# Optimization experiments

Hardware: AMD Instinct MI355X
Metric: run time of the kernel (lower is better)

## Reference

```python
import jax, jax.numpy as jnp
import numpy as np

X_DIM, R_DIM, U_DIM, V_DIM, H_DIM = 64, 64, 64, 64, 128


def setup_inputs() -> dict:
    key = jax.random.key(0)
    k1, k2, k3, k4, k5 = jax.random.split(key, 5)
    n, i, j = 8, 32, 32
    r = jax.random.normal(k1, (n, i, j, R_DIM), dtype=jnp.float32)
    u = jax.random.normal(k2, (n, R_DIM, U_DIM, V_DIM), dtype=jnp.float32)
    v = jax.random.normal(k3, (n, i, j, V_DIM), dtype=jnp.float32)
    # xavier_uniform scaling: gain=1, fan computed over last two dims per torch default
    def xavier(k, shape):
        fan_in, fan_out = shape[-1], shape[-2]
        # torch xavier on >2D tensor: fan_in = shape[1]*prod(shape[2:]), fan_out = shape[0]*prod(shape[2:])
        rf = int(np.prod(shape[2:])) if len(shape) > 2 else 1
        fi = shape[1] * rf
        fo = shape[0] * rf
        bound = float(np.sqrt(6.0 / (fi + fo)))
        return jax.random.uniform(k, shape, dtype=jnp.float32, minval=-bound, maxval=bound)
    w1 = xavier(k4, (R_DIM, U_DIM, V_DIM, H_DIM))
    w2 = xavier(k5, (X_DIM, R_DIM, H_DIM))
    return {"r": r, "u": u, "v": v, "w1": w1, "w2": w2}


def reference(r, u, v, w1, w2):
    # contract w1 with u over (u_dim, v_dim) -> per-batch tensor a[n, r, v', h]
    # original: einsum('ruvh,nruv,nijv->nijrh')
    a = jnp.einsum('ruvh,nruv->nrvh', w1, u)          # contract u axis; v survives? no:
    # Careful: in 'ruvh,nruv,nijv->nijrh', v is contracted across all three.
    # Do it in two GEMM-friendly steps: first contract u-axis, keeping v.
    # a: [n, r, v, h] (contracted only over u)
    a = jnp.einsum('ruvh,nruv->nrvh', w1, u)
    # then contract v with v-tensor: [n,i,j,v] x [n,r,v,h] -> [n,i,j,r,h]
    x = jax.nn.relu(jnp.einsum('nijv,nrvh->nijrh', v, a))
    # second einsum: 'xrh,nijr,nijrh->nijx'
    # fuse r-weighting into x first (elementwise over r), then contract (r,h) with w2
    out = jnp.einsum('xrh,nijrh->nijx', w2, x * r[..., None])
    return out
```

## Files before the change

### kernel.cpp

```cpp
#include <hip/hip_runtime.h>
#include <hip/hip_bf16.h>

#define RD 64
#define UD 64
#define VD 64
#define HD 128
#define XD 64
#define NB 8
#define SITES 1024

typedef float f32x4 __attribute__((ext_vector_type(4)));
typedef float f32x2 __attribute__((ext_vector_type(2)));
typedef __bf16 bf16x4 __attribute__((ext_vector_type(4)));
typedef __bf16 bf16x8 __attribute__((ext_vector_type(8)));
typedef unsigned int u32x4 __attribute__((ext_vector_type(4)));
typedef unsigned short u16;
typedef unsigned short u16x4 __attribute__((ext_vector_type(4)));

__device__ __forceinline__ void lds_barrier() {
  __builtin_amdgcn_s_waitcnt(0xC07F);
  __builtin_amdgcn_s_barrier();
}

__global__ void kprep(const float* __restrict__ w2, u16* __restrict__ w2t,
                      const float* __restrict__ r, float* __restrict__ rt,
                      const float* __restrict__ u, float* __restrict__ ut) {
  __shared__ float tl[64][68];
  int b = blockIdx.x;
  int t = threadIdx.x;
  if (b < 256) {
    int rr = b >> 2, qq = b & 3;
    for (int i = 0; i < 8; ++i) {
      int idx = qq * 2048 + i * 256 + t;
      int x = idx >> 7, h = idx & 127;
      float val = w2[((size_t)x * RD + rr) * HD + h];
      __hip_bfloat16 hv = __float2bfloat16(val);
      w2t[((size_t)rr * XD + x) * HD + h] = *(u16*)&hv;
    }
  } else if (b < 384) {
    int bb = b - 256;
    int n = bb >> 4, sb = (bb & 15) * 64;
    for (int i = 0; i < 4; ++i) {
      int flat = i * 256 + t;
      int s = flat >> 4, ch = flat & 15;
      f32x4 d = *(const f32x4*)(r + ((size_t)(n * SITES + sb + s) * RD + ch * 4));
      *(f32x4*)&tl[s][ch * 4] = d;
    }
    __syncthreads();
    for (int i = 0; i < 4; ++i) {
      int flat = i * 256 + t;
      int rr = flat >> 4, ch = flat & 15;
      f32x4 o;
      o.x = tl[ch * 4 + 0][rr];
      o.y = tl[ch * 4 + 1][rr];
      o.z = tl[ch * 4 + 2][rr];
      o.w = tl[ch * 4 + 3][rr];
      *(f32x4*)(rt + ((size_t)(n * RD + rr) * SITES + sb + ch * 4)) = o;
    }
  } else {
    int f = (b - 384) * 256 + t;
    int nh = f & 1, v = (f >> 1) & 63, uu = (f >> 7) & 63, rr = f >> 13;
    f32x4 o;
#pragma unroll
    for (int k = 0; k < 4; ++k)
      o[k] = u[(((size_t)(nh * 4 + k) * RD + rr) * UD + uu) * VD + v];
    *(f32x4*)(ut + (size_t)f * 4) = o;
  }
}

#define PF 4
__global__ __launch_bounds__(512, 4) void k_a_full(const float* __restrict__ w1,
                                                   const float* __restrict__ ut,
                                                   u16* __restrict__ at) {
  __shared__ float red[256 * 32];
  __shared__ float tile[8 * 32 * 33];
  int b = blockIdx.x;
  int rr = b >> 3, vh = (b >> 2) & 1, hb = b & 3;
  int t = threadIdx.x;
  int uh = t >> 8;
  int L = t & 255;
  int vl = L >> 3, hs = L & 7;
  int v = vh * 32 + vl;
  int h0 = hb * 32 + hs * 4;
  const float* w1p = w1 + (((size_t)(rr * UD + uh * 32)) * VD + v) * HD + h0;
  const float* up  = ut + (((size_t)(rr * UD + uh * 32)) * VD + v) * NB;
  const size_t wstep = (size_t)VD * HD;
  const size_t ustep = (size_t)VD * NB;

  f32x4 acc[8];
#pragma unroll
  for (int n = 0; n < 8; ++n) acc[n] = (f32x4)0.f;

  f32x4 wa[PF], ua[PF], ub[PF];
#pragma unroll
  for (int p = 0; p < PF; ++p) {
    wa[p] = *(const f32x4*)(w1p + (size_t)p * wstep);
    ua[p] = *(const f32x4*)(up + (size_t)p * ustep);
    ub[p] = *(const f32x4*)(up + (size_t)p * ustep + 4);
  }
#pragma unroll
  for (int uu = 0; uu < 32; ++uu) {
    const int p = uu & (PF - 1);
    f32x4 wv = wa[p];
    f32x4 a0 = ua[p];
    f32x4 a1 = ub[p];
    if (uu + PF < 32) {
      wa[p] = *(const f32x4*)(w1p + (size_t)(uu + PF) * wstep);
      ua[p] = *(const f32x4*)(up + (size_t)(uu + PF) * ustep);
      ub[p] = *(const f32x4*)(up + (size_t)(uu + PF) * ustep + 4);
    }
    acc[0] += wv * a0.x;
    acc[1] += wv * a0.y;
    acc[2] += wv * a0.z;
    acc[3] += wv * a0.w;
    acc[4] += wv * a1.x;
    acc[5] += wv * a1.y;
    acc[6] += wv * a1.z;
    acc[7] += wv * a1.w;
  }

  if (uh == 1) {
#pragma unroll
    for (int n = 0; n < 8; ++n)
      *(f32x4*)&red[L * 32 + ((n ^ (L & 7)) << 2)] = acc[n];
  }
  __syncthreads();
  if (uh == 0) {
#pragma unroll
    for (int n = 0; n < 8; ++n)
      acc[n] += *(const f32x4*)&red[L * 32 + ((n ^ (L & 7)) << 2)];
#pragma unroll
    for (int n = 0; n < 8; ++n)
#pragma unroll
      for (int j = 0; j < 4; ++j)
        tile[(n * 32 + hs * 4 + j) * 33 + vl] = acc[n][j];
  }
  __syncthreads();

#pragma unroll
  for (int k = 0; k < 4; ++k) {
    int flat = k * 512 + t;
    int vs = flat & 7, hl = (flat >> 3) & 31, n = flat >> 8;
    f32x4 blk = *(const f32x4*)&tile[(n * 32 + hl) * 33 + vs * 4];
    u16x4 o;
#pragma unroll
    for (int j = 0; j < 4; ++j) {
      __hip_bfloat16 hv = __float2bfloat16(blk[j]);
      o[j] = *(u16*)&hv;
    }
    *(u16x4*)(at + ((size_t)(n * RD + rr) * HD + hb * 32 + hl) * VD + vh * 32 + vs * 4) = o;
  }
}

__global__ __launch_bounds__(256, 1) void k_main(const float* __restrict__ vin,
                                                 const u16* __restrict__ at,
                                                 const u16* __restrict__ w2t,
                                                 const float* __restrict__ rt,
                                                 float* __restrict__ pbuf) {
  __shared__ __align__(16) char Plds[2 * 128 * 256];
  int b = blockIdx.x;
  int rc = b & 7, st = (b >> 3) & 7, n = b >> 6;
  int t = threadIdx.x;
  int w = t >> 6, L = t & 63, q = L >> 4, c = L & 15;
  int g2m = w >> 1, g2x = w & 1;

  bf16x8 vf[4][2];
#pragma unroll
  for (int nt = 0; nt < 4; ++nt)
#pragma unroll
    for (int ks = 0; ks < 2; ++ks) {
      int s = (w & 1) * 64 + nt * 16 + c;
      const float* vp = vin + ((size_t)(n * SITES + st * 128 + s) * VD + ks * 32 + q * 8);
      f32x4 a0 = *(const f32x4*)vp;
      f32x4 a1 = *(const f32x4*)(vp + 4);
      bf16x8 f;
      f[0] = (__bf16)a0.x; f[1] = (__bf16)a0.y; f[2] = (__bf16)a0.z; f[3] = (__bf16)a0.w;
      f[4] = (__bf16)a1.x; f[5] = (__bf16)a1.y; f[6] = (__bf16)a1.z; f[7] = (__bf16)a1.w;
      vf[nt][ks] = f;
    }

  f32x4 o[4][2];
#pragma unroll
  for (int i = 0; i < 4; i++)
#pragma unroll
    for (int j = 0; j < 2; j++) o[i][j] = (f32x4)0.f;

  int g1m = w >> 1, g1n = w & 1;
  for (int rr = rc * 8; rr < rc * 8 + 8; ++rr) {
    const u16* abase = at + (size_t)(n * RD + rr) * 8192;

    bf16x8 af[4][2];
#pragma unroll
    for (int mt = 0; mt < 4; ++mt)
#pragma unroll
      for (int ks = 0; ks < 2; ++ks) {
        int h = g1m * 64 + mt * 16 + c;
        int vb = ks * 4 + q;
        af[mt][ks] = *(const bf16x8*)(abase + (size_t)h * VD + vb * 8);
      }
    u32x4 wraw[2][4];
#pragma unroll
    for (int xt = 0; xt < 2; ++xt)
#pragma unroll
      for (int k2 = 0; k2 < 4; ++k2) {
        int xg = g2x * 32 + xt * 16 + c;
        wraw[xt][k2] = *(const u32x4*)((const char*)w2t +
                        (((size_t)(rr * XD + xg)) * HD + k2 * 32 + q * 8) * 2);
      }
    float rsc[4];
#pragma unroll
    for (int nt = 0; nt < 4; ++nt)
      rsc[nt] = rt[(size_t)(n * RD + rr) * SITES + st * 128 + g1n * 64 + nt * 16 + c];

    f32x4 cc[4][4];
#pragma unroll
    for (int mt = 0; mt < 4; ++mt)
#pragma unroll
      for (int nt = 0; nt < 4; ++nt) cc[mt][nt] = (f32x4)0.f;
#pragma unroll
    for (int ks = 0; ks < 2; ++ks)
#pragma unroll
      for (int mt = 0; mt < 4; ++mt)
#pragma unroll
        for (int nt = 0; nt < 4; ++nt)
          cc[mt][nt] = __builtin_amdgcn_mfma_f32_16x16x32_bf16(af[mt][ks], vf[nt][ks],
                                                               cc[mt][nt], 0, 0, 0);

    char* PB = Plds + (rr & 1) * 32768;
#pragma unroll
    for (int mt = 0; mt < 4; ++mt)
#pragma unroll
      for (int nt = 0; nt < 4; ++nt) {
        float sc = rsc[nt];
        bf16x4 pv;
#pragma unroll
        for (int jj = 0; jj < 4; ++jj) {
          float x = cc[mt][nt][jj];
          x = x > 0.f ? x : 0.f;
          pv[jj] = (__bf16)(x * sc);
        }
        int s = g1n * 64 + nt * 16 + c;
        int blk = g1m * 8 + mt * 2 + (q >> 1);
        *(bf16x4*)(PB + (size_t)s * 256 + (size_t)((blk ^ c) * 16 + (q & 1) * 8)) = pv;
      }
    lds_barrier();

#pragma unroll
    for (int k2 = 0; k2 < 4; ++k2) {
      bf16x8 wf0 = __builtin_bit_cast(bf16x8, wraw[0][k2]);
      bf16x8 wf1 = __builtin_bit_cast(bf16x8, wraw[1][k2]);
#pragma unroll
      for (int mt = 0; mt < 4; ++mt) {
        int s = g2m * 64 + mt * 16 + c;
        int blk = k2 * 4 + q;
        bf16x8 pf = *(const bf16x8*)(PB + (size_t)s * 256 + (size_t)((blk ^ c) * 16));
        o[mt][0] = __builtin_amdgcn_mfma_f32_16x16x32_bf16(pf, wf0, o[mt][0], 0, 0, 0);
        o[mt][1] = __builtin_amdgcn_mfma_f32_16x16x32_bf16(pf, wf1, o[mt][1], 0, 0, 0);
      }
    }
  }
#pragma unroll
  for (int mt = 0; mt < 4; ++mt)
#pragma unroll
    for (int xt = 0; xt < 2; ++xt) {
      int s0 = g2m * 64 + mt * 16 + q * 4;
      int x = g2x * 32 + xt * 16 + c;
      size_t off = ((((size_t)rc * NB + n) * 8 + st) * XD + x) * 128 + s0;
      *(f32x4*)(pbuf + off) = o[mt][xt];
    }
}

__global__ __launch_bounds__(256) void k_reduce(const float* __restrict__ pbuf,
                                                float* __restrict__ out) {
  __shared__ float tile[128][17];
  int b = blockIdx.x;
  int n = b >> 5, st = (b >> 2) & 7, xq = b & 3;
  int t = threadIdx.x;
  int sq = t & 31, xl = t >> 5;
#pragma unroll
  for (int p = 0; p < 2; ++p) {
    int x = xq * 16 + p * 8 + xl;
    f32x4 sum = (f32x4)0.f;
#pragma unroll
    for (int rcc = 0; rcc < 8; ++rcc) {
      size_t off = ((((size_t)rcc * NB + n) * 8 + st) * XD + x) * 128 + sq * 4;
      f32x4 d = *(const f32x4*)(pbuf + off);
      sum.x += d.x; sum.y += d.y; sum.z += d.z; sum.w += d.w;
    }
#pragma unroll
    for (int k = 0; k < 4; ++k) tile[sq * 4 + k][p * 8 + xl] = sum[k];
  }
  __syncthreads();
#pragma unroll
  for (int k = 0; k < 2; ++k) {
    int flat = k * 256 + t;
    int s = flat >> 2, c4 = flat & 3;
    f32x4 o;
#pragma unroll
    for (int j = 0; j < 4; ++j) o[j] = tile[s][c4 * 4 + j];
    *(f32x4*)(out + ((size_t)(n * SITES + st * 128 + s) * XD + xq * 16 + c4 * 4)) = o;
  }
}

extern "C" void kernel_launch(void* const* d_in, const int* in_sizes, int n_in,
                              void* d_out, int out_size, void* d_ws, size_t ws_size,
                              hipStream_t stream) {
  const float* r  = (const float*)d_in[0];
  const float* u  = (const float*)d_in[1];
  const float* v  = (const float*)d_in[2];
  const float* w1 = (const float*)d_in[3];
  const float* w2 = (const float*)d_in[4];
  float* out = (float*)d_out;
  char* ws = (char*)d_ws;
  u16* at     = (u16*)(ws);
  u16* w2t    = (u16*)(ws + ((size_t)8 << 20));
  float* rt   = (float*)(ws + ((size_t)9 << 20));
  float* ut   = (float*)(ws + ((size_t)11 << 20));
  float* pbuf = (float*)(ws + ((size_t)19 << 20));

  hipLaunchKernelGGL(kprep, dim3(2432), dim3(256), 0, stream, w2, w2t, r, rt, u, ut);
  hipLaunchKernelGGL(k_a_full, dim3(512), dim3(512), 0, stream, w1, ut, at);
  hipLaunchKernelGGL(k_main, dim3(512), dim3(256), 0, stream, v, at, w2t, rt, pbuf);
  hipLaunchKernelGGL(k_reduce, dim3(256), dim3(256), 0, stream, pbuf, out);
}
```

Measured before the change: 255.3 us.

## Stage u slab in shared memory inside k_a_full instead of pre-transposing

```diff
diff --git a/kernel.cpp b/kernel.cpp
--- a/kernel.cpp
+++ b/kernel.cpp
@@ -23,8 +23,7 @@
 }
 
 __global__ void kprep(const float* __restrict__ w2, u16* __restrict__ w2t,
-                      const float* __restrict__ r, float* __restrict__ rt,
-                      const float* __restrict__ u, float* __restrict__ ut) {
+                      const float* __restrict__ r, float* __restrict__ rt) {
   __shared__ float tl[64][68];
   int b = blockIdx.x;
   int t = threadIdx.x;
@@ -37,7 +36,7 @@
       __hip_bfloat16 hv = __float2bfloat16(val);
       w2t[((size_t)rr * XD + x) * HD + h] = *(u16*)&hv;
     }
-  } else if (b < 384) {
+  } else {
     int bb = b - 256;
     int n = bb >> 4, sb = (bb & 15) * 64;
     for (int i = 0; i < 4; ++i) {
@@ -57,23 +56,14 @@
       o.w = tl[ch * 4 + 3][rr];
       *(f32x4*)(rt + ((size_t)(n * RD + rr) * SITES + sb + ch * 4)) = o;
     }
-  } else {
-    int f = (b - 384) * 256 + t;
-    int nh = f & 1, v = (f >> 1) & 63, uu = (f >> 7) & 63, rr = f >> 13;
-    f32x4 o;
-#pragma unroll
-    for (int k = 0; k < 4; ++k)
-      o[k] = u[(((size_t)(nh * 4 + k) * RD + rr) * UD + uu) * VD + v];
-    *(f32x4*)(ut + (size_t)f * 4) = o;
   }
 }
 
 #define PF 4
 __global__ __launch_bounds__(512, 4) void k_a_full(const float* __restrict__ w1,
-                                                   const float* __restrict__ ut,
+                                                   const float* __restrict__ u,
                                                    u16* __restrict__ at) {
-  __shared__ float red[256 * 32];
-  __shared__ float tile[8 * 32 * 33];
+  __shared__ __align__(16) float smem[16640];
   int b = blockIdx.x;
   int rr = b >> 3, vh = (b >> 2) & 1, hb = b & 3;
   int t = threadIdx.x;
@@ -82,43 +72,50 @@
   int vl = L >> 3, hs = L & 7;
   int v = vh * 32 + vl;
   int h0 = hb * 32 + hs * 4;
+
+  {
+    const float* ub = u + (size_t)rr * UD * VD + (size_t)vh * 32;
+#pragma unroll
+    for (int i = 0; i < 8; ++i) {
+      int s = i * 512 + t;
+      int n = s >> 9, uu = (s >> 3) & 63, vg = s & 7;
+      f32x4 d = *(const f32x4*)(ub + (size_t)n * (RD * UD * VD) + (size_t)uu * VD + vg * 4);
+      *(f32x4*)&smem[s * 4] = d;
+    }
+  }
+  __syncthreads();
+
   const float* w1p = w1 + (((size_t)(rr * UD + uh * 32)) * VD + v) * HD + h0;
-  const float* up  = ut + (((size_t)(rr * UD + uh * 32)) * VD + v) * NB;
   const size_t wstep = (size_t)VD * HD;
-  const size_t ustep = (size_t)VD * NB;
+  const float* uslab = smem + (size_t)uh * 32 * 32 + vl;
 
   f32x4 acc[8];
 #pragma unroll
   for (int n = 0; n < 8; ++n) acc[n] = (f32x4)0.f;
 
-  f32x4 wa[PF], ua[PF], ub[PF];
-#pragma unroll
-  for (int p = 0; p < PF; ++p) {
-    wa[p] = *(const f32x4*)(w1p + (size_t)p * wstep);
-    ua[p] = *(const f32x4*)(up + (size_t)p * ustep);
-    ub[p] = *(const f32x4*)(up + (size_t)p * ustep + 4);
-  }
-#pragma unroll
-  for (int uu = 0; uu < 32; ++uu) {
-    const int p = uu & (PF - 1);
+  f32x4 wa[PF];
+#pragma unroll
+  for (int p = 0; p < PF; ++p) wa[p] = *(const f32x4*)(w1p + (size_t)p * wstep);
+#pragma unroll
+  for (int uul = 0; uul < 32; ++uul) {
+    const int p = uul & (PF - 1);
     f32x4 wv = wa[p];
-    f32x4 a0 = ua[p];
-    f32x4 a1 = ub[p];
-    if (uu + PF < 32) {
-      wa[p] = *(const f32x4*)(w1p + (size_t)(uu + PF) * wstep);
-      ua[p] = *(const f32x4*)(up + (size_t)(uu + PF) * ustep);
-      ub[p] = *(const f32x4*)(up + (size_t)(uu + PF) * ustep + 4);
-    }
-    acc[0] += wv * a0.x;
-    acc[1] += wv * a0.y;
-    acc[2] += wv * a0.z;
-    acc[3] += wv * a0.w;
-    acc[4] += wv * a1.x;
-    acc[5] += wv * a1.y;
-    acc[6] += wv * a1.z;
-    acc[7] += wv * a1.w;
-  }
-
+    if (uul + PF < 32) wa[p] = *(const f32x4*)(w1p + (size_t)(uul + PF) * wstep);
+    const float* up = uslab + (size_t)uul * 32;
+    acc[0] += wv * up[0 * 2048];
+    acc[1] += wv * up[1 * 2048];
+    acc[2] += wv * up[2 * 2048];
+    acc[3] += wv * up[3 * 2048];
+    acc[4] += wv * up[4 * 2048];
+    acc[5] += wv * up[5 * 2048];
+    acc[6] += wv * up[6 * 2048];
+    acc[7] += wv * up[7 * 2048];
+  }
+
+  __syncthreads();
+
+  float* red  = smem;
+  float* tile = smem + 8192;
   if (uh == 1) {
 #pragma unroll
     for (int n = 0; n < 8; ++n)
@@ -315,11 +312,10 @@
   u16* at     = (u16*)(ws);
   u16* w2t    = (u16*)(ws + ((size_t)8 << 20));
   float* rt   = (float*)(ws + ((size_t)9 << 20));
-  float* ut   = (float*)(ws + ((size_t)11 << 20));
   float* pbuf = (float*)(ws + ((size_t)19 << 20));
 
-  hipLaunchKernelGGL(kprep, dim3(2432), dim3(256), 0, stream, w2, w2t, r, rt, u, ut);
-  hipLaunchKernelGGL(k_a_full, dim3(512), dim3(512), 0, stream, w1, ut, at);
+  hipLaunchKernelGGL(kprep, dim3(384), dim3(256), 0, stream, w2, w2t, r, rt);
+  hipLaunchKernelGGL(k_a_full, dim3(512), dim3(512), 0, stream, w1, u, at);
   hipLaunchKernelGGL(k_main, dim3(512), dim3(256), 0, stream, v, at, w2t, rt, pbuf);
   hipLaunchKernelGGL(k_reduce, dim3(256), dim3(256), 0, stream, pbuf, out);
 }
```

After: 261.0 us. +2.2%, slower.
